# Performance work log

Measured on AMD Instinct MI355X. Metric: run time of the kernel, lower is better.

Reference implementation:

```python
import jax, jax.numpy as jnp
import numpy as np

LN_EPS = 1e-5


def setup_inputs() -> dict:
    key = jax.random.key(0)
    ks = jax.random.split(key, 4)
    B, N, H, HEADS = 2, 1024, 64, 8
    road_vectors = jax.random.normal(ks[0], (B, N, 4), dtype=jnp.float32) * 10.0
    W1 = jax.random.normal(ks[1], (5, H), dtype=jnp.float32) * (1.0 / np.sqrt(5.0))
    b1 = jnp.zeros((H,), dtype=jnp.float32)
    ln_gamma = jnp.ones((H,), dtype=jnp.float32)
    ln_beta = jnp.zeros((H,), dtype=jnp.float32)
    W2 = jax.random.normal(ks[2], (H, HEADS), dtype=jnp.float32) * (1.0 / np.sqrt(H))
    b2 = jnp.zeros((HEADS,), dtype=jnp.float32)
    return {"road_vectors": road_vectors, "W1": W1, "b1": b1,
            "ln_gamma": ln_gamma, "ln_beta": ln_beta, "W2": W2, "b2": b2}


def reference(road_vectors, W1, b1, ln_gamma, ln_beta, W2, b2):
    start = road_vectors[..., 0:2]                      # [B,N,2]
    end = road_vectors[..., 2:4]
    vec = end - start
    headings = jnp.arctan2(vec[..., 1], vec[..., 0])    # [B,N]
    # pairwise [B,N,N]: index i along axis 1, j along axis 2
    delta_heading = headings[:, :, None] - headings[:, None, :]
    feat_cos = jnp.cos(delta_heading)
    feat_sin = jnp.sin(delta_heading)
    delta_pos = start[:, :, None, :] - start[:, None, :, :]  # [B,N,N,2]
    dist = jnp.linalg.norm(delta_pos, axis=-1)
    feat_dist = jnp.log(dist + 1e-5)
    h_i = headings[:, :, None]                           # broadcast over j
    c = jnp.cos(h_i)
    s = jnp.sin(h_i)
    dx = delta_pos[..., 0]
    dy = delta_pos[..., 1]
    feat_rel_x = dx * c + dy * s
    feat_rel_y = -dx * s + dy * c
    geom = jnp.stack([feat_dist, feat_cos, feat_sin, feat_rel_x, feat_rel_y], axis=-1)  # [B,N,N,5]
    h = jnp.einsum('bijf,fh->bijh', geom, W1) + b1       # [B,N,N,64]
    mu = jnp.mean(h, axis=-1, keepdims=True)
    var = jnp.mean(jnp.square(h - mu), axis=-1, keepdims=True)
    h = (h - mu) / jnp.sqrt(var + LN_EPS) * ln_gamma + ln_beta
    h = jax.nn.relu(h)
    bias = jnp.einsum('bijh,hk->bijk', h, W2) + b2       # [B,N,N,heads]
    return jnp.transpose(bias, (0, 3, 1, 2))             # [B,heads,N,N]
```

## Files before the change

### kernel.cpp

```cpp
#include <hip/hip_runtime.h>
#include <math.h>

#define NB 2
#define NN 1024
#define NH 64
#define NK 8
#define ITILE 8

typedef float f32x2 __attribute__((ext_vector_type(2)));
typedef float f32x16 __attribute__((ext_vector_type(16)));
typedef _Float16 half8 __attribute__((ext_vector_type(8)));
typedef _Float16 half2t __attribute__((ext_vector_type(2)));
typedef __fp16 fp16x2 __attribute__((ext_vector_type(2)));
typedef unsigned u32x2 __attribute__((ext_vector_type(2)));

union FragU { uint32_t u[4]; uint4 q; half8 h; };
union H2U  { half2t h; fp16x2 p; uint32_t u; };
union C32U { f32x16 v; f32x2 d[8]; float f[16]; };

static __device__ __forceinline__ uint32_t pk_rne(float a, float b) {
    half2t t; t[0] = (_Float16)a; t[1] = (_Float16)b;
    H2U r; r.h = t; return r.u;
}

static __device__ __forceinline__ void half_swap(uint32_t a, uint32_t b,
                                                 uint32_t& w0, uint32_t& w2) {
#if __has_builtin(__builtin_amdgcn_permlane32_swap)
    u32x2 s = __builtin_amdgcn_permlane32_swap(a, b, false, false);
    w0 = s[0]; w2 = s[1];
#else
    const int hi = (threadIdx.x & 63) >> 5;
    uint32_t pa = __shfl_xor(a, 32), pb = __shfl_xor(b, 32);
    w0 = hi ? pb : a;
    w2 = hi ? b : pa;
#endif
}

static __device__ __forceinline__ float wave_sum_half(float v) {
#if __has_builtin(__builtin_amdgcn_permlane32_swap)
    union { float f; uint32_t u; } a, r0, r1;
    a.f = v;
    u32x2 s = __builtin_amdgcn_permlane32_swap(a.u, a.u, false, false);
    r0.u = s[0]; r1.u = s[1];
    return r0.f + r1.f;
#else
    return v + __shfl_xor(v, 32);
#endif
}

__global__ void prep_kernel(const float* __restrict__ rv,
                            const float* __restrict__ W1,
                            const float* __restrict__ b1,
                            const float* __restrict__ W2,
                            const float* __restrict__ gamma,
                            const float* __restrict__ beta,
                            float* __restrict__ pt,
                            float* __restrict__ w1tab,
                            uint4* __restrict__ w2pack,
                            uint2* __restrict__ gbtab,
                            int* __restrict__ flagp) {
    const int tid = threadIdx.x;
    const int bid = blockIdx.x;
    if (bid < 8) {
        const int idx = bid * 256 + tid;
        const float x0 = rv[idx*4+0], y0 = rv[idx*4+1];
        const float vx = rv[idx*4+2] - x0, vy = rv[idx*4+3] - y0;
        const float rinv = rsqrtf(fmaf(vx, vx, vy * vy));
        float4 o; o.x = x0; o.y = y0; o.z = vx * rinv; o.w = vy * rinv;
        reinterpret_cast<float4*>(pt)[idx] = o;
    } else {
        __shared__ float mean[6];
        __shared__ int oks;
        if (tid == 0) oks = 1;
        if (tid < 5)       { float m = 0.f; for (int h = 0; h < NH; ++h) m += W1[tid*NH+h]; mean[tid] = m * (1.f/NH); }
        else if (tid == 5) { float m = 0.f; for (int h = 0; h < NH; ++h) m += b1[h];        mean[5]   = m * (1.f/NH); }
        __syncthreads();
        if (tid < NH) {
            const int h = tid;
            w1tab[h*8+0] = W1[0*NH+h]-mean[0];
            w1tab[h*8+1] = W1[1*NH+h]-mean[1];
            w1tab[h*8+2] = W1[2*NH+h]-mean[2];
            w1tab[h*8+3] = W1[3*NH+h]-mean[3];
            w1tab[h*8+4] = W1[4*NH+h]-mean[4];
            w1tab[h*8+5] = b1[h]-mean[5];
            w1tab[h*8+6] = 0.f;
            w1tab[h*8+7] = 0.f;
            if (!(beta[h] == 0.f && gamma[h] >= 0.f)) atomicAnd(&oks, 0);
        }
        __syncthreads();
        const int fast = oks;
        if (tid == 0) *flagp = fast;
        {
            const int c = tid >> 6, l = tid & 63;
            const int row = l & 31;
            const int hb = 16*c + 8*(l >> 5);
            uint32_t dw[4];
            for (int t = 0; t < 4; ++t) {
                const int h0 = hb + 2*t;
                const float gA = fast ? gamma[h0]   : 1.f;
                const float gB = fast ? gamma[h0+1] : 1.f;
                const float a = (row < 8) ? W2[h0*NK + row] * gA     : 0.f;
                const float d = (row < 8) ? W2[(h0+1)*NK + row] * gB : 0.f;
                dw[t] = pk_rne(a, d);
            }
            uint4 v; v.x = dw[0]; v.y = dw[1]; v.z = dw[2]; v.w = dw[3];
            w2pack[c*64 + l] = v;
        }
        if (tid < 32) {
            const int hig = tid >> 4, m16 = tid & 15;
            const int T = m16 >> 3, m = m16 & 7;
            const int h0 = 32*T + 8*(m>>1) + 2*(m&1) + 4*hig;
            uint2 gb;
            gb.x = pk_rne(gamma[h0], gamma[h0+1]);
            gb.y = pk_rne(beta[h0],  beta[h0+1]);
            gbtab[hig*16 + m16] = gb;
        }
    }
}

__global__ __launch_bounds__(256, 4) void rpe_kernel(
    const float* __restrict__ pt,
    const float* __restrict__ w1tab,
    const uint4* __restrict__ w2pack,
    const uint2* __restrict__ gbtab,
    const int* __restrict__ flagp,
    const float* __restrict__ b2,
    float* __restrict__ out) {
    __shared__ uint4 qlds[ITILE * 2 * 64];
    const int tid  = threadIdx.x;
    const int wave = tid >> 6;
    const int lane = tid & 63;
    const int jj   = lane & 31;
    const int hi   = lane >> 5;
    const int b  = blockIdx.z;
    const int j0 = blockIdx.x * 128 + wave * 32;
    const int iBase = blockIdx.y * ITILE;

    const float4* pt4 = reinterpret_cast<const float4*>(pt);
    const float4* ptb = pt4 + b*NN + iBase;

    {
        const int it = tid >> 5;
        const int sl = tid & 31;
        const float4 p = ptb[it];
        const float x0 = p.x, y0 = p.y, ci = p.z, si = p.w;
        const float u1 = fmaf(x0, ci, y0 * si);
        const float u2 = fmaf(y0, ci, -x0 * si);
        const float4* t4 = reinterpret_cast<const float4*>(w1tab);
#pragma unroll
        for (int T = 0; T < 2; ++T) {
            const int h = 32*T + sl;
            const float4 ra = t4[h*2];
            const float4 rb = t4[h*2+1];
            const float qc = fmaf(ra.y, ci,  ra.z * si);
            const float qs = fmaf(ra.y, si, -ra.z * ci);
            const float qx = fmaf(-ra.w, ci,  rb.x * si);
            const float qy = fmaf(-ra.w, si, -rb.x * ci);
            const float cn = fmaf(ra.w, u1, fmaf(rb.x, u2, rb.y));
            H2U a_, b_, c_;
            a_.p = __builtin_amdgcn_cvt_pkrtz(qc, qs);
            b_.p = __builtin_amdgcn_cvt_pkrtz(qx, qy);
            c_.p = __builtin_amdgcn_cvt_pkrtz(ra.x, cn);
            uint4 v; v.x = a_.u; v.y = b_.u; v.z = c_.u; v.w = 0u;
            qlds[(it*2+T)*64 + sl]      = v;
            qlds[(it*2+T)*64 + 32 + sl] = make_uint4(0,0,0,0);
        }
    }
    __syncthreads();

    const float4 pj = pt4[b*NN + j0 + jj];
    const float xj = pj.x, yj = pj.y;
    H2U d0u, d1u;
    d0u.p = __builtin_amdgcn_cvt_pkrtz(pj.z, pj.w);
    d1u.p = __builtin_amdgcn_cvt_pkrtz(xj, yj);
    const uint32_t d0 = d0u.u, d1 = d1u.u;

    FragU a2[4];
#pragma unroll
    for (int c = 0; c < 4; ++c) a2[c].q = w2pack[c*64 + lane];
    float b2v[4];
#pragma unroll
    for (int r = 0; r < 4; ++r) b2v[r] = b2[4*hi + r];

    const f32x16 z16 = {0,0,0,0,0,0,0,0,0,0,0,0,0,0,0,0};
    half2t z2h; z2h[0] = (_Float16)0.f; z2h[1] = (_Float16)0.f;
    const size_t plane = (size_t)NN * NN;
    float* o0 = out + (size_t)(b*NK + 4*hi)*plane + (size_t)iBase*NN + (j0 + jj);
    float* o1 = o0 + plane;
    float* o2 = o0 + 2*plane;
    float* o3 = o0 + 3*plane;

    const int fast = *flagp;

    if (fast) {
        for (int ii = 0; ii < ITILE; ++ii) {
            FragU qf0, qf1;
            qf0.q = qlds[(ii*2+0)*64 + lane];
            qf1.q = qlds[(ii*2+1)*64 + lane];
            const float4 piv = ptb[ii];

            const float dx = piv.x - xj, dy = piv.y - yj;
            const float dist = __builtin_amdgcn_sqrtf(fmaf(dx, dx, dy * dy));
            const float g32 = 0.69314718f * __builtin_amdgcn_logf(dist + 1e-5f);
            H2U e0; e0.p = __builtin_amdgcn_cvt_pkrtz(g32, 1.0f);
            FragU bf; bf.u[0] = d0; bf.u[1] = d1; bf.u[2] = e0.u; bf.u[3] = 0u;

            __builtin_amdgcn_s_setprio(1);
            C32U cA, cB;
            cA.v = __builtin_amdgcn_mfma_f32_32x32x16_f16(qf0.h, bf.h, z16, 0, 0, 0);
            cB.v = __builtin_amdgcn_mfma_f32_32x32x16_f16(qf1.h, bf.h, z16, 0, 0, 0);
            __builtin_amdgcn_s_setprio(0);

            f32x2 q0 = cA.d[0]*cA.d[0], q1 = cA.d[1]*cA.d[1], q2 = cA.d[2]*cA.d[2], q3 = cA.d[3]*cA.d[3];
            q0 = __builtin_elementwise_fma(cA.d[4], cA.d[4], q0);
            q1 = __builtin_elementwise_fma(cA.d[5], cA.d[5], q1);
            q2 = __builtin_elementwise_fma(cA.d[6], cA.d[6], q2);
            q3 = __builtin_elementwise_fma(cA.d[7], cA.d[7], q3);
            q0 = __builtin_elementwise_fma(cB.d[0], cB.d[0], q0);
            q1 = __builtin_elementwise_fma(cB.d[1], cB.d[1], q1);
            q2 = __builtin_elementwise_fma(cB.d[2], cB.d[2], q2);
            q3 = __builtin_elementwise_fma(cB.d[3], cB.d[3], q3);
            q0 = __builtin_elementwise_fma(cB.d[4], cB.d[4], q0);
            q1 = __builtin_elementwise_fma(cB.d[5], cB.d[5], q1);
            q2 = __builtin_elementwise_fma(cB.d[6], cB.d[6], q2);
            q3 = __builtin_elementwise_fma(cB.d[7], cB.d[7], q3);
            q0 += q1; q2 += q3; q0 += q2;
            float sq = q0[0] + q0[1];
            sq = wave_sum_half(sq);
            const float inv = __builtin_amdgcn_rsqf(fmaf(sq, 1.f/64.f, 1e-5f));

            uint32_t yw[16];
#pragma unroll
            for (int m = 0; m < 8; ++m) {
                H2U t; t.p = __builtin_amdgcn_cvt_pkrtz(cA.d[m][0], cA.d[m][1]);
                half2t r = __builtin_elementwise_max(t.h, z2h);
                H2U o; o.h = r; yw[m] = o.u;
            }
#pragma unroll
            for (int m = 0; m < 8; ++m) {
                H2U t; t.p = __builtin_amdgcn_cvt_pkrtz(cB.d[m][0], cB.d[m][1]);
                half2t r = __builtin_elementwise_max(t.h, z2h);
                H2U o; o.h = r; yw[8+m] = o.u;
            }

            C32U acc0, acc1;
            acc0.v = z16; acc1.v = z16;
            __builtin_amdgcn_s_setprio(1);
#pragma unroll
            for (int c = 0; c < 2; ++c) {
                uint32_t w0, w1, w2, w3;
                half_swap(yw[4*c + 0], yw[4*c + 2], w0, w2);
                half_swap(yw[4*c + 1], yw[4*c + 3], w1, w3);
                FragU Bf; Bf.u[0] = w0; Bf.u[1] = w1; Bf.u[2] = w2; Bf.u[3] = w3;
                acc0.v = __builtin_amdgcn_mfma_f32_32x32x16_f16(a2[c].h, Bf.h, acc0.v, 0, 0, 0);
            }
#pragma unroll
            for (int c = 2; c < 4; ++c) {
                uint32_t w0, w1, w2, w3;
                half_swap(yw[4*c + 0], yw[4*c + 2], w0, w2);
                half_swap(yw[4*c + 1], yw[4*c + 3], w1, w3);
                FragU Bf; Bf.u[0] = w0; Bf.u[1] = w1; Bf.u[2] = w2; Bf.u[3] = w3;
                acc1.v = __builtin_amdgcn_mfma_f32_32x32x16_f16(a2[c].h, Bf.h, acc1.v, 0, 0, 0);
            }
            __builtin_amdgcn_s_setprio(0);

            o0[0] = fmaf(acc0.f[0] + acc1.f[0], inv, b2v[0]);
            o1[0] = fmaf(acc0.f[1] + acc1.f[1], inv, b2v[1]);
            o2[0] = fmaf(acc0.f[2] + acc1.f[2], inv, b2v[2]);
            o3[0] = fmaf(acc0.f[3] + acc1.f[3], inv, b2v[3]);
            o0 += NN; o1 += NN; o2 += NN; o3 += NN;
        }
    } else {
        for (int ii = 0; ii < ITILE; ++ii) {
            FragU qf0, qf1;
            qf0.q = qlds[(ii*2+0)*64 + lane];
            qf1.q = qlds[(ii*2+1)*64 + lane];
            const float4 piv = ptb[ii];

            const float dx = piv.x - xj, dy = piv.y - yj;
            const float dist = __builtin_amdgcn_sqrtf(fmaf(dx, dx, dy * dy));
            const float g32 = 0.69314718f * __builtin_amdgcn_logf(dist + 1e-5f);
            H2U e0; e0.p = __builtin_amdgcn_cvt_pkrtz(g32, 1.0f);
            FragU bf; bf.u[0] = d0; bf.u[1] = d1; bf.u[2] = e0.u; bf.u[3] = 0u;

            C32U cA, cB;
            cA.v = __builtin_amdgcn_mfma_f32_32x32x16_f16(qf0.h, bf.h, z16, 0, 0, 0);
            cB.v = __builtin_amdgcn_mfma_f32_32x32x16_f16(qf1.h, bf.h, z16, 0, 0, 0);

            f32x2 q0 = cA.d[0]*cA.d[0], q1 = cA.d[1]*cA.d[1], q2 = cA.d[2]*cA.d[2], q3 = cA.d[3]*cA.d[3];
            q0 = __builtin_elementwise_fma(cA.d[4], cA.d[4], q0);
            q1 = __builtin_elementwise_fma(cA.d[5], cA.d[5], q1);
            q2 = __builtin_elementwise_fma(cA.d[6], cA.d[6], q2);
            q3 = __builtin_elementwise_fma(cA.d[7], cA.d[7], q3);
            q0 = __builtin_elementwise_fma(cB.d[0], cB.d[0], q0);
            q1 = __builtin_elementwise_fma(cB.d[1], cB.d[1], q1);
            q2 = __builtin_elementwise_fma(cB.d[2], cB.d[2], q2);
            q3 = __builtin_elementwise_fma(cB.d[3], cB.d[3], q3);
            q0 = __builtin_elementwise_fma(cB.d[4], cB.d[4], q0);
            q1 = __builtin_elementwise_fma(cB.d[5], cB.d[5], q1);
            q2 = __builtin_elementwise_fma(cB.d[6], cB.d[6], q2);
            q3 = __builtin_elementwise_fma(cB.d[7], cB.d[7], q3);
            q0 += q1; q2 += q3; q0 += q2;
            float sq = q0[0] + q0[1];
            sq = wave_sum_half(sq);
            const float inv = __builtin_amdgcn_rsqf(fmaf(sq, 1.f/64.f, 1e-5f));
            H2U inv2u; inv2u.p = __builtin_amdgcn_cvt_pkrtz(inv, inv);
            const half2t inv2 = inv2u.h;

            uint32_t yw[16];
#pragma unroll
            for (int m = 0; m < 16; ++m) {
                const f32x2 src = (m < 8) ? cA.d[m] : cB.d[m - 8];
                uint2 gb = gbtab[hi*16 + m];
                H2U x; x.p = __builtin_amdgcn_cvt_pkrtz(src[0], src[1]);
                H2U gg, bb; gg.u = gb.x; bb.u = gb.y;
                half2t gs = gg.h * inv2;
                half2t y = __builtin_elementwise_fma(x.h, gs, bb.h);
                y = __builtin_elementwise_max(y, z2h);
                H2U o; o.h = y; yw[m] = o.u;
            }

            C32U acc0, acc1;
            acc0.v = z16; acc1.v = z16;
#pragma unroll
            for (int c = 0; c < 2; ++c) {
                uint32_t w0, w1, w2, w3;
                half_swap(yw[4*c + 0], yw[4*c + 2], w0, w2);
                half_swap(yw[4*c + 1], yw[4*c + 3], w1, w3);
                FragU Bf; Bf.u[0] = w0; Bf.u[1] = w1; Bf.u[2] = w2; Bf.u[3] = w3;
                acc0.v = __builtin_amdgcn_mfma_f32_32x32x16_f16(a2[c].h, Bf.h, acc0.v, 0, 0, 0);
            }
#pragma unroll
            for (int c = 2; c < 4; ++c) {
                uint32_t w0, w1, w2, w3;
                half_swap(yw[4*c + 0], yw[4*c + 2], w0, w2);
                half_swap(yw[4*c + 1], yw[4*c + 3], w1, w3);
                FragU Bf; Bf.u[0] = w0; Bf.u[1] = w1; Bf.u[2] = w2; Bf.u[3] = w3;
                acc1.v = __builtin_amdgcn_mfma_f32_32x32x16_f16(a2[c].h, Bf.h, acc1.v, 0, 0, 0);
            }

            o0[0] = acc0.f[0] + acc1.f[0] + b2v[0];
            o1[0] = acc0.f[1] + acc1.f[1] + b2v[1];
            o2[0] = acc0.f[2] + acc1.f[2] + b2v[2];
            o3[0] = acc0.f[3] + acc1.f[3] + b2v[3];
            o0 += NN; o1 += NN; o2 += NN; o3 += NN;
        }
    }
}

extern "C" void kernel_launch(void* const* d_in, const int* in_sizes, int n_in,
                              void* d_out, int out_size, void* d_ws, size_t ws_size,
                              hipStream_t stream) {
    const float* rv    = (const float*)d_in[0];
    const float* W1    = (const float*)d_in[1];
    const float* b1    = (const float*)d_in[2];
    const float* gamma = (const float*)d_in[3];
    const float* beta  = (const float*)d_in[4];
    const float* W2    = (const float*)d_in[5];
    const float* b2    = (const float*)d_in[6];
    float* out = (float*)d_out;

    float* ws = (float*)d_ws;
    float* pt     = ws;
    float* w1tab  = ws + 8192;
    uint4* w2pack = (uint4*)(ws + 8704);
    uint2* gbtab  = (uint2*)(ws + 9728);
    int*   flagp  = (int*)(ws + 9792);

    prep_kernel<<<9, 256, 0, stream>>>(rv, W1, b1, W2, gamma, beta,
                                       pt, w1tab, w2pack, gbtab, flagp);

    dim3 grid(NN / 128, NN / ITILE, NB);
    rpe_kernel<<<grid, 256, 0, stream>>>(pt, w1tab, w2pack, gbtab, flagp, b2, out);
}
```

Before: 32.27 us.

## Fold prep kernel into main kernel, recompute weight tables per block

Removes the separate prep kernel launch and workspace round-trip. Each block now computes the W1 column means, the gamma/beta fast-path flag, the gamma-scaled W2 MFMA fragments and the per-point unit headings directly from the raw inputs, using shared memory and wave shuffles. This removes one launch and the dependency between two kernels. In exchange, every one of 2048 blocks repeats the weight preprocessing and adds extra barriers before its main loop.

```diff
diff --git a/kernel.cpp b/kernel.cpp
--- a/kernel.cpp
+++ b/kernel.cpp
@@ -48,85 +48,21 @@
 #endif
 }
 
-__global__ void prep_kernel(const float* __restrict__ rv,
-                            const float* __restrict__ W1,
-                            const float* __restrict__ b1,
-                            const float* __restrict__ W2,
-                            const float* __restrict__ gamma,
-                            const float* __restrict__ beta,
-                            float* __restrict__ pt,
-                            float* __restrict__ w1tab,
-                            uint4* __restrict__ w2pack,
-                            uint2* __restrict__ gbtab,
-                            int* __restrict__ flagp) {
-    const int tid = threadIdx.x;
-    const int bid = blockIdx.x;
-    if (bid < 8) {
-        const int idx = bid * 256 + tid;
-        const float x0 = rv[idx*4+0], y0 = rv[idx*4+1];
-        const float vx = rv[idx*4+2] - x0, vy = rv[idx*4+3] - y0;
-        const float rinv = rsqrtf(fmaf(vx, vx, vy * vy));
-        float4 o; o.x = x0; o.y = y0; o.z = vx * rinv; o.w = vy * rinv;
-        reinterpret_cast<float4*>(pt)[idx] = o;
-    } else {
-        __shared__ float mean[6];
-        __shared__ int oks;
-        if (tid == 0) oks = 1;
-        if (tid < 5)       { float m = 0.f; for (int h = 0; h < NH; ++h) m += W1[tid*NH+h]; mean[tid] = m * (1.f/NH); }
-        else if (tid == 5) { float m = 0.f; for (int h = 0; h < NH; ++h) m += b1[h];        mean[5]   = m * (1.f/NH); }
-        __syncthreads();
-        if (tid < NH) {
-            const int h = tid;
-            w1tab[h*8+0] = W1[0*NH+h]-mean[0];
-            w1tab[h*8+1] = W1[1*NH+h]-mean[1];
-            w1tab[h*8+2] = W1[2*NH+h]-mean[2];
-            w1tab[h*8+3] = W1[3*NH+h]-mean[3];
-            w1tab[h*8+4] = W1[4*NH+h]-mean[4];
-            w1tab[h*8+5] = b1[h]-mean[5];
-            w1tab[h*8+6] = 0.f;
-            w1tab[h*8+7] = 0.f;
-            if (!(beta[h] == 0.f && gamma[h] >= 0.f)) atomicAnd(&oks, 0);
-        }
-        __syncthreads();
-        const int fast = oks;
-        if (tid == 0) *flagp = fast;
-        {
-            const int c = tid >> 6, l = tid & 63;
-            const int row = l & 31;
-            const int hb = 16*c + 8*(l >> 5);
-            uint32_t dw[4];
-            for (int t = 0; t < 4; ++t) {
-                const int h0 = hb + 2*t;
-                const float gA = fast ? gamma[h0]   : 1.f;
-                const float gB = fast ? gamma[h0+1] : 1.f;
-                const float a = (row < 8) ? W2[h0*NK + row] * gA     : 0.f;
-                const float d = (row < 8) ? W2[(h0+1)*NK + row] * gB : 0.f;
-                dw[t] = pk_rne(a, d);
-            }
-            uint4 v; v.x = dw[0]; v.y = dw[1]; v.z = dw[2]; v.w = dw[3];
-            w2pack[c*64 + l] = v;
-        }
-        if (tid < 32) {
-            const int hig = tid >> 4, m16 = tid & 15;
-            const int T = m16 >> 3, m = m16 & 7;
-            const int h0 = 32*T + 8*(m>>1) + 2*(m&1) + 4*hig;
-            uint2 gb;
-            gb.x = pk_rne(gamma[h0], gamma[h0+1]);
-            gb.y = pk_rne(beta[h0],  beta[h0+1]);
-            gbtab[hig*16 + m16] = gb;
-        }
-    }
-}
-
 __global__ __launch_bounds__(256, 4) void rpe_kernel(
-    const float* __restrict__ pt,
-    const float* __restrict__ w1tab,
-    const uint4* __restrict__ w2pack,
-    const uint2* __restrict__ gbtab,
-    const int* __restrict__ flagp,
+    const float* __restrict__ rv,
+    const float* __restrict__ W1,
+    const float* __restrict__ b1,
+    const float* __restrict__ W2,
+    const float* __restrict__ gamma,
+    const float* __restrict__ beta,
     const float* __restrict__ b2,
     float* __restrict__ out) {
     __shared__ uint4 qlds[ITILE * 2 * 64];
+    __shared__ float w1t[NH][6];
+    __shared__ float w2g[NH * NK];
+    __shared__ float meanS[6];
+    __shared__ int oks;
+
     const int tid  = threadIdx.x;
     const int wave = tid >> 6;
     const int lane = tid & 63;
@@ -136,31 +72,81 @@
     const int j0 = blockIdx.x * 128 + wave * 32;
     const int iBase = blockIdx.y * ITILE;
 
-    const float4* pt4 = reinterpret_cast<const float4*>(pt);
-    const float4* ptb = pt4 + b*NN + iBase;
+    const float4* rv4 = reinterpret_cast<const float4*>(rv);
+    const float4* rvb = rv4 + b*NN + iBase;
+
+    if (tid == 0) oks = 1;
+    {
+        float m1 = (wave < 4) ? W1[wave*NH + lane] : 0.f;
+#pragma unroll
+        for (int off = 1; off < 64; off <<= 1) m1 += __shfl_xor(m1, off);
+        if (lane == 0 && wave < 4) meanS[wave] = m1 * (1.f/NH);
+        float m2 = 0.f;
+        if (wave == 0) m2 = W1[4*NH + lane];
+        else if (wave == 1) m2 = b1[lane];
+#pragma unroll
+        for (int off = 1; off < 64; off <<= 1) m2 += __shfl_xor(m2, off);
+        if (lane == 0 && wave == 0) meanS[4] = m2 * (1.f/NH);
+        if (lane == 0 && wave == 1) meanS[5] = m2 * (1.f/NH);
+    }
+    __syncthreads();
+    if (tid < NH) {
+        if (!(beta[tid] == 0.f && gamma[tid] >= 0.f)) atomicAnd(&oks, 0);
+    }
+    __syncthreads();
+    const int fast = oks;
+    if (tid < NH) {
+        const int h = tid;
+        const float gh = fast ? gamma[h] : 1.f;
+#pragma unroll
+        for (int k = 0; k < NK; ++k) w2g[h*NK + k] = W2[h*NK + k] * gh;
+        w1t[h][0] = W1[0*NH+h] - meanS[0];
+        w1t[h][1] = W1[1*NH+h] - meanS[1];
+        w1t[h][2] = W1[2*NH+h] - meanS[2];
+        w1t[h][3] = W1[3*NH+h] - meanS[3];
+        w1t[h][4] = W1[4*NH+h] - meanS[4];
+        w1t[h][5] = b1[h] - meanS[5];
+    }
+    __syncthreads();
+
+    FragU a2[4];
+#pragma unroll
+    for (int c = 0; c < 4; ++c) {
+        const int row = lane & 31;
+        const int hb = 16*c + 8*(lane >> 5);
+#pragma unroll
+        for (int t = 0; t < 4; ++t) {
+            const int h0 = hb + 2*t;
+            const float a = (row < 8) ? w2g[h0*NK + row]     : 0.f;
+            const float d = (row < 8) ? w2g[(h0+1)*NK + row] : 0.f;
+            a2[c].u[t] = pk_rne(a, d);
+        }
+    }
 
     {
         const int it = tid >> 5;
         const int sl = tid & 31;
-        const float4 p = ptb[it];
-        const float x0 = p.x, y0 = p.y, ci = p.z, si = p.w;
+        const float4 p = rvb[it];
+        const float x0 = p.x, y0 = p.y;
+        const float vx = p.z - x0, vy = p.w - y0;
+        const float rinv = rsqrtf(fmaf(vx, vx, vy * vy));
+        const float ci = vx * rinv, si = vy * rinv;
         const float u1 = fmaf(x0, ci, y0 * si);
         const float u2 = fmaf(y0, ci, -x0 * si);
-        const float4* t4 = reinterpret_cast<const float4*>(w1tab);
 #pragma unroll
         for (int T = 0; T < 2; ++T) {
             const int h = 32*T + sl;
-            const float4 ra = t4[h*2];
-            const float4 rb = t4[h*2+1];
-            const float qc = fmaf(ra.y, ci,  ra.z * si);
-            const float qs = fmaf(ra.y, si, -ra.z * ci);
-            const float qx = fmaf(-ra.w, ci,  rb.x * si);
-            const float qy = fmaf(-ra.w, si, -rb.x * ci);
-            const float cn = fmaf(ra.w, u1, fmaf(rb.x, u2, rb.y));
+            const float w0v = w1t[h][0], w1v = w1t[h][1], w2v = w1t[h][2];
+            const float w3v = w1t[h][3], w4v = w1t[h][4], bbc = w1t[h][5];
+            const float qc = fmaf(w1v, ci,  w2v * si);
+            const float qs = fmaf(w1v, si, -w2v * ci);
+            const float qx = fmaf(-w3v, ci,  w4v * si);
+            const float qy = fmaf(-w3v, si, -w4v * ci);
+            const float cn = fmaf(w3v, u1, fmaf(w4v, u2, bbc));
             H2U a_, b_, c_;
             a_.p = __builtin_amdgcn_cvt_pkrtz(qc, qs);
             b_.p = __builtin_amdgcn_cvt_pkrtz(qx, qy);
-            c_.p = __builtin_amdgcn_cvt_pkrtz(ra.x, cn);
+            c_.p = __builtin_amdgcn_cvt_pkrtz(w0v, cn);
             uint4 v; v.x = a_.u; v.y = b_.u; v.z = c_.u; v.w = 0u;
             qlds[(it*2+T)*64 + sl]      = v;
             qlds[(it*2+T)*64 + 32 + sl] = make_uint4(0,0,0,0);
@@ -168,16 +154,15 @@
     }
     __syncthreads();
 
-    const float4 pj = pt4[b*NN + j0 + jj];
+    const float4 pj = rv4[b*NN + j0 + jj];
     const float xj = pj.x, yj = pj.y;
+    const float vxj = pj.z - xj, vyj = pj.w - yj;
+    const float rinvj = rsqrtf(fmaf(vxj, vxj, vyj * vyj));
     H2U d0u, d1u;
-    d0u.p = __builtin_amdgcn_cvt_pkrtz(pj.z, pj.w);
+    d0u.p = __builtin_amdgcn_cvt_pkrtz(vxj * rinvj, vyj * rinvj);
     d1u.p = __builtin_amdgcn_cvt_pkrtz(xj, yj);
     const uint32_t d0 = d0u.u, d1 = d1u.u;
 
-    FragU a2[4];
-#pragma unroll
-    for (int c = 0; c < 4; ++c) a2[c].q = w2pack[c*64 + lane];
     float b2v[4];
 #pragma unroll
     for (int r = 0; r < 4; ++r) b2v[r] = b2[4*hi + r];
@@ -190,14 +175,12 @@
     float* o2 = o0 + 2*plane;
     float* o3 = o0 + 3*plane;
 
-    const int fast = *flagp;
-
     if (fast) {
         for (int ii = 0; ii < ITILE; ++ii) {
             FragU qf0, qf1;
             qf0.q = qlds[(ii*2+0)*64 + lane];
             qf1.q = qlds[(ii*2+1)*64 + lane];
-            const float4 piv = ptb[ii];
+            const float4 piv = rvb[ii];
 
             const float dx = piv.x - xj, dy = piv.y - yj;
             const float dist = __builtin_amdgcn_sqrtf(fmaf(dx, dx, dy * dy));
@@ -275,7 +258,7 @@
             FragU qf0, qf1;
             qf0.q = qlds[(ii*2+0)*64 + lane];
             qf1.q = qlds[(ii*2+1)*64 + lane];
-            const float4 piv = ptb[ii];
+            const float4 piv = rvb[ii];
 
             const float dx = piv.x - xj, dy = piv.y - yj;
             const float dist = __builtin_amdgcn_sqrtf(fmaf(dx, dx, dy * dy));
@@ -311,9 +294,12 @@
 #pragma unroll
             for (int m = 0; m < 16; ++m) {
                 const f32x2 src = (m < 8) ? cA.d[m] : cB.d[m - 8];
-                uint2 gb = gbtab[hi*16 + m];
+                const int T = m >> 3, mm = m & 7;
+                const int h0 = 32*T + 8*(mm>>1) + 2*(mm&1) + 4*hi;
                 H2U x; x.p = __builtin_amdgcn_cvt_pkrtz(src[0], src[1]);
-                H2U gg, bb; gg.u = gb.x; bb.u = gb.y;
+                H2U gg, bb;
+                gg.u = pk_rne(gamma[h0], gamma[h0+1]);
+                bb.u = pk_rne(beta[h0],  beta[h0+1]);
                 half2t gs = gg.h * inv2;
                 half2t y = __builtin_elementwise_fma(x.h, gs, bb.h);
                 y = __builtin_elementwise_max(y, z2h);
@@ -360,16 +346,6 @@
     const float* b2    = (const float*)d_in[6];
     float* out = (float*)d_out;
 
-    float* ws = (float*)d_ws;
-    float* pt     = ws;
-    float* w1tab  = ws + 8192;
-    uint4* w2pack = (uint4*)(ws + 8704);
-    uint2* gbtab  = (uint2*)(ws + 9728);
-    int*   flagp  = (int*)(ws + 9792);
-
-    prep_kernel<<<9, 256, 0, stream>>>(rv, W1, b1, W2, gamma, beta,
-                                       pt, w1tab, w2pack, gbtab, flagp);
-
     dim3 grid(NN / 128, NN / ITILE, NB);
-    rpe_kernel<<<grid, 256, 0, stream>>>(pt, w1tab, w2pack, gbtab, flagp, b2, out);
-}
+    rpe_kernel<<<grid, 256, 0, stream>>>(rv, W1, b1, W2, gamma, beta, b2, out);
+}
```

New measurement: 30.89 us. 4.3% less time.
